# Kernel optimization log

Measured on AMD Instinct MI355X. Metric: run time of the kernel, lower is better.

Reference implementation:

```python
import jax, jax.numpy as jnp
import numpy as np

N = 100000   # nodes
E = 1600000  # edges
IN = 128     # input feature dim
C = 64       # per-layer output dim (filters)
H = 2        # attention heads
EPS = 1e-5   # batchnorm eps


def setup_inputs() -> dict:
    key = jax.random.key(0)
    ks = jax.random.split(key, 32)
    rn = lambda k, s, sc=0.05: jax.random.normal(k, s, jnp.float32) * sc
    inp = {
        "x": jax.random.normal(ks[0], (N, IN), jnp.float32),
        "edge_index": jax.random.randint(ks[1], (2, E), 0, N, jnp.int32),
        # GATConv layer 0 (IN -> C, H heads, concat=False)
        "W0": rn(ks[2], (IN, H * C)), "as0": rn(ks[3], (H, C)), "ad0": rn(ks[4], (H, C)), "b0": jnp.zeros((C,), jnp.float32),
        "skip0": rn(ks[5], (IN, C)),  # Linear(IN->C, bias=False); layers 1,2 skips are Identity
        "g0": jnp.ones((C,), jnp.float32), "be0": jnp.zeros((C,), jnp.float32),
        # GATConv layer 1 (C -> C)
        "W1": rn(ks[6], (C, H * C)), "as1": rn(ks[7], (H, C)), "ad1": rn(ks[8], (H, C)), "b1": jnp.zeros((C,), jnp.float32),
        "g1": jnp.ones((C,), jnp.float32), "be1": jnp.zeros((C,), jnp.float32),
        # GATConv layer 2 (C -> C)
        "W2": rn(ks[9], (C, H * C)), "as2": rn(ks[10], (H, C)), "ad2": rn(ks[11], (H, C)), "b2": jnp.zeros((C,), jnp.float32),
        "g2": jnp.ones((C,), jnp.float32), "be2": jnp.zeros((C,), jnp.float32),
        # JK projection for input (IN -> C, with bias); other projections are Identity
        "projW": rn(ks[12], (IN, C)), "projb": jnp.zeros((C,), jnp.float32),
    }
    return inp


def _gat(x, edge_index, W, a_src, a_dst, b):
    # PyG GATConv, concat=False: mean over heads, bias added after mean.
    h = (x @ W).reshape(-1, H, C)                 # [N, H, C]
    src, dst = edge_index[0], edge_index[1]
    e_src = jnp.sum(h * a_src, axis=-1)           # [N, H]
    e_dst = jnp.sum(h * a_dst, axis=-1)           # [N, H]
    e = jax.nn.leaky_relu(e_src[src] + e_dst[dst], 0.2)  # [E, H]
    m = jax.ops.segment_max(e, dst, num_segments=N)      # neighbor softmax (stable)
    w = jnp.exp(e - m[dst])
    denom = jax.ops.segment_sum(w, dst, num_segments=N)
    alpha = w / (denom[dst] + 1e-16)              # [E, H]
    out = jax.ops.segment_sum(alpha[:, :, None] * h[src], dst, num_segments=N)  # [N, H, C]
    return out.mean(axis=1) + b


def _bn(x, g, b):
    # BatchNorm1d, training-mode batch statistics (deterministic reference)
    mu = x.mean(axis=0)
    var = x.var(axis=0)
    return (x - mu) * jax.lax.rsqrt(var + EPS) * g + b


def reference(x, edge_index, W0, as0, ad0, b0, skip0, g0, be0,
              W1, as1, ad1, b1, g1, be1,
              W2, as2, ad2, b2, g2, be2,
              projW, projb):
    lrelu = lambda v: jax.nn.leaky_relu(v, 0.01)  # nn.LeakyReLU default
    jk0 = x @ projW + projb                       # proj_lyrs[0]
    # layer 0: GAT + projected skip, BN, (dropout=identity in eval), LeakyReLU
    h1 = _gat(x, edge_index, W0, as0, ad0, b0) + x @ skip0
    h1 = lrelu(_bn(h1, g0, be0))
    # layer 1: identity skip
    h2 = _gat(h1, edge_index, W1, as1, ad1, b1) + h1
    h2 = lrelu(_bn(h2, g1, be1))
    # layer 2: identity skip
    h3 = _gat(h2, edge_index, W2, as2, ad2, b2) + h2
    h3 = lrelu(_bn(h3, g2, be2))
    # jumping knowledge, mode='max': elementwise max over [input_proj, h1, h2, h3]
    return jnp.max(jnp.stack([jk0, h1, h2, h3], axis=0), axis=0)
```

## Files before the change

### kernel.cpp

```cpp
#include <hip/hip_runtime.h>

#define NN 100000
#define NE 1600000

constexpr int NBUC = 196;
constexpr int BIN_CHUNK = 4096;
constexpr int NB_BIN = (NE + BIN_CHUNK - 1) / BIN_CHUNK;

typedef __attribute__((ext_vector_type(8))) short s16x8;
typedef __attribute__((ext_vector_type(4))) float f32x4;
typedef __attribute__((ext_vector_type(2))) float f32x2;

__device__ inline unsigned short f2bf(float f) {
    unsigned int u = __float_as_uint(f);
    return (unsigned short)((u + 0x7fffu + ((u >> 16) & 1u)) >> 16);
}
__device__ inline float bf_lo(unsigned int pk) { return __uint_as_float(pk << 16); }
__device__ inline float bf_hi(unsigned int pk) { return __uint_as_float(pk & 0xffff0000u); }

__global__ void zero_u32(unsigned int* p, int n) {
    int i = blockIdx.x * blockDim.x + threadIdx.x;
    if (i < n) p[i] = 0u;
}

__global__ __launch_bounds__(256) void bucket_count(const int* __restrict__ dst,
                                                    int* __restrict__ bcount) {
    __shared__ int hist[NBUC];
    int t = threadIdx.x;
    for (int b = t; b < NBUC; b += 256) hist[b] = 0;
    __syncthreads();
    int beg = blockIdx.x * BIN_CHUNK;
    int end = min(beg + BIN_CHUNK, NE);
    for (int i = beg + t; i < end; i += 256) atomicAdd(&hist[dst[i] >> 9], 1);
    __syncthreads();
    for (int b = t; b < NBUC; b += 256)
        if (hist[b]) atomicAdd(&bcount[b], hist[b]);
}

__global__ void bucket_scan(const int* __restrict__ bcount, int* __restrict__ bbase,
                            int* __restrict__ bucket_cursor, int* __restrict__ offsets) {
    if (threadIdx.x == 0) {
        int run = 0;
        for (int b = 0; b < NBUC; ++b) {
            bbase[b] = run;
            bucket_cursor[b] = run;
            run += bcount[b];
        }
        bbase[NBUC] = NE;
        offsets[NN] = NE;
    }
}

__global__ __launch_bounds__(256) void bin_edges(const int* __restrict__ src,
                                                 const int* __restrict__ dst,
                                                 int* __restrict__ bucket_cursor,
                                                 unsigned int* __restrict__ binned) {
    __shared__ int hist[NBUC];
    __shared__ int base[NBUC];
    int t = threadIdx.x;
    for (int b = t; b < NBUC; b += 256) hist[b] = 0;
    __syncthreads();
    int beg = blockIdx.x * BIN_CHUNK;
    int end = min(beg + BIN_CHUNK, NE);
    for (int i = beg + t; i < end; i += 256) atomicAdd(&hist[dst[i] >> 9], 1);
    __syncthreads();
    for (int b = t; b < NBUC; b += 256) {
        base[b] = hist[b] ? atomicAdd(&bucket_cursor[b], hist[b]) : 0;
        hist[b] = 0;
    }
    __syncthreads();
    for (int i = beg + t; i < end; i += 256) {
        int d = dst[i];
        int bk = d >> 9;
        int loc = atomicAdd(&hist[bk], 1);
        binned[base[bk] + loc] = ((unsigned)(d & 511) << 17) | (unsigned)src[i];
    }
}

__global__ __launch_bounds__(256) void bucket_sort(const unsigned int* __restrict__ binned,
                                                   const int* __restrict__ bbase,
                                                   int* __restrict__ offsets,
                                                   int* __restrict__ csr_src,
                                                   int* __restrict__ csr_dst) {
    __shared__ int deg[512];
    __shared__ int loc[512];
    __shared__ int s2[256];
    int t = threadIdx.x;
    int b = blockIdx.x;
    int beg = bbase[b], end = bbase[b + 1];
    int nbase = b << 9;
    deg[t] = 0;
    deg[t + 256] = 0;
    __syncthreads();
    for (int i = beg + t; i < end; i += 256) atomicAdd(&deg[binned[i] >> 17], 1);
    __syncthreads();
    int pairsum = deg[2 * t] + deg[2 * t + 1];
    s2[t] = pairsum;
    __syncthreads();
    for (int off = 1; off < 256; off <<= 1) {
        int v = (t >= off) ? s2[t - off] : 0;
        __syncthreads();
        s2[t] += v;
        __syncthreads();
    }
    int ex = s2[t] - pairsum;
    loc[2 * t] = ex;
    loc[2 * t + 1] = ex + deg[2 * t];
    __syncthreads();
    for (int i = t; i < 512; i += 256) {
        int node = nbase + i;
        if (node < NN) offsets[node] = beg + loc[i];
    }
    __syncthreads();
    for (int i = beg + t; i < end; i += 256) {
        unsigned int v = binned[i];
        int dl = v >> 17;
        int pos = atomicAdd(&loc[dl], 1);
        csr_src[beg + pos] = (int)(v & 0x1FFFFu);
        csr_dst[beg + pos] = nbase + dl;
    }
}

__global__ void prep_weights(const float* __restrict__ W0, const float* __restrict__ skip0,
                             const float* __restrict__ projW, const float* __restrict__ W1,
                             const float* __restrict__ W2, unsigned short* __restrict__ Wtcat,
                             unsigned short* __restrict__ Wt1, unsigned short* __restrict__ Wt2) {
    int i = blockIdx.x * 256 + threadIdx.x;
    if (i < 32768) {
        int oc = i >> 7, k = i & 127;
        float v;
        if (oc < 128) v = W0[k * 128 + oc];
        else if (oc < 192) v = skip0[k * 64 + (oc - 128)];
        else v = projW[k * 64 + (oc - 192)];
        Wtcat[oc * 128 + k] = f2bf(v);
    } else if (i < 40960) {
        int j = i - 32768, oc = j >> 6, k = j & 63;
        Wt1[oc * 64 + k] = f2bf(W1[k * 128 + oc]);
    } else if (i < 49152) {
        int j = i - 40960, oc = j >> 6, k = j & 63;
        Wt2[oc * 64 + k] = f2bf(W2[k * 128 + oc]);
    }
}

template <int K, bool L0, bool XFORM>
__global__ __launch_bounds__(256) void gemm_mfma(
    const float* __restrict__ X, const unsigned short* __restrict__ Wt,
    unsigned int* __restrict__ Hq32, float* __restrict__ skipx, float* __restrict__ jkproj,
    const float* __restrict__ projb, const float* __restrict__ bnsc,
    const float* __restrict__ as_v, const float* __restrict__ ad_v,
    unsigned int* __restrict__ e_srcpk, unsigned int* __restrict__ e_dstpk) {
    constexpr int KP = K + 8;
    __shared__ unsigned short As[64 * KP];
    __shared__ unsigned short Bs[128 * KP];
    int t = threadIdx.x;
    int rbase = blockIdx.x * 64;
    const unsigned short* Wtg = Wt + (size_t)blockIdx.y * 128 * K;

    for (int i = t; i < 64 * (K / 4); i += 256) {
        int r = i / (K / 4);
        int kq = (i % (K / 4)) * 4;
        int gr = rbase + r;
        float4 v = make_float4(0.f, 0.f, 0.f, 0.f);
        if (gr < NN) {
            v = *(const float4*)&X[(size_t)gr * K + kq];
            if (XFORM) {
                float* vc = (float*)&v;
#pragma unroll
                for (int c = 0; c < 4; ++c) {
                    float val = vc[c] * bnsc[kq + c] + bnsc[64 + kq + c];
                    vc[c] = val >= 0.f ? val : 0.01f * val;
                }
            }
        }
        uint2 u;
        u.x = (unsigned int)f2bf(v.x) | ((unsigned int)f2bf(v.y) << 16);
        u.y = (unsigned int)f2bf(v.z) | ((unsigned int)f2bf(v.w) << 16);
        *(uint2*)&As[r * KP + kq] = u;
    }
    for (int i = t; i < 128 * (K / 8); i += 256) {
        int oc = i / (K / 8);
        int k8 = (i % (K / 8)) * 8;
        uint4 v = *(const uint4*)&Wtg[(size_t)oc * K + k8];
        *(uint4*)&Bs[oc * KP + k8] = v;
    }
    __syncthreads();

    int lane = t & 63, wv = t >> 6;
    int lr = lane & 15, quad = lane >> 4;
    int arow = wv * 16 + lr;
    f32x4 acc[8];
#pragma unroll
    for (int c = 0; c < 8; ++c) acc[c] = (f32x4)(0.f);
#pragma unroll
    for (int k0 = 0; k0 < K; k0 += 32) {
        s16x8 a = *(const s16x8*)&As[arow * KP + k0 + quad * 8];
#pragma unroll
        for (int ct = 0; ct < 8; ++ct) {
            s16x8 b = *(const s16x8*)&Bs[(ct * 16 + lr) * KP + k0 + quad * 8];
            acc[ct] = __builtin_amdgcn_mfma_f32_16x16x32_bf16(a, b, acc[ct], 0, 0, 0);
        }
    }

    bool hblock = (!L0) || (blockIdx.y == 0);
#pragma unroll
    for (int reg = 0; reg < 4; ++reg) {
        int row = rbase + wv * 16 + quad * 4 + reg;
        if (hblock) {
            if (row < NN) {
#pragma unroll
                for (int ct = 0; ct < 4; ++ct) {
                    int pk = __builtin_amdgcn_cvt_pk_fp8_f32(acc[ct][reg], acc[ct + 4][reg],
                                                             0, false);
                    int pn = __shfl_xor(pk, 1, 64);
                    if (!(lr & 1))
                        Hq32[(size_t)row * 32 + ct * 8 + (lr >> 1)] =
                            (unsigned int)((pk & 0xFFFF) | (pn << 16));
                }
            }
            float s0 = 0.f, s1 = 0.f, d0 = 0.f, d1 = 0.f;
#pragma unroll
            for (int ct = 0; ct < 4; ++ct) {
                int c = ct * 16 + lr;
                float hlo = acc[ct][reg], hhi = acc[ct + 4][reg];
                s0 += hlo * as_v[c];
                s1 += hhi * as_v[64 + c];
                d0 += hlo * ad_v[c];
                d1 += hhi * ad_v[64 + c];
            }
#pragma unroll
            for (int off = 1; off < 16; off <<= 1) {
                s0 += __shfl_xor(s0, off, 64);
                s1 += __shfl_xor(s1, off, 64);
                d0 += __shfl_xor(d0, off, 64);
                d1 += __shfl_xor(d1, off, 64);
            }
            if (lr == 0 && row < NN) {
                e_srcpk[row] = (unsigned int)f2bf(s0) | ((unsigned int)f2bf(s1) << 16);
                e_dstpk[row] = (unsigned int)f2bf(d0) | ((unsigned int)f2bf(d1) << 16);
            }
        } else if (row < NN) {
#pragma unroll
            for (int ct = 0; ct < 4; ++ct)
                skipx[(size_t)row * 64 + ct * 16 + lr] = acc[ct][reg];
#pragma unroll
            for (int ct = 4; ct < 8; ++ct) {
                int c = (ct - 4) * 16 + lr;
                jkproj[(size_t)row * 64 + c] = acc[ct][reg] + projb[c];
            }
        }
    }
}

__global__ void edge_w(const int* __restrict__ csr_src, const int* __restrict__ csr_dst,
                       const unsigned int* __restrict__ e_srcpk,
                       const unsigned int* __restrict__ e_dstpk,
                       uint2* __restrict__ erec) {
    int i = blockIdx.x * blockDim.x + threadIdx.x;
    if (i >= NE) return;
    int s = csr_src[i];
    unsigned int q = e_srcpk[s];
    unsigned int r = e_dstpk[csr_dst[i]];
    float a0 = bf_lo(q) + bf_lo(r);
    float a1 = bf_hi(q) + bf_hi(r);
    a0 = a0 >= 0.f ? a0 : 0.2f * a0;
    a1 = a1 >= 0.f ? a1 : 0.2f * a1;
    unsigned int w = (unsigned int)f2bf(__expf(a0)) | ((unsigned int)f2bf(__expf(a1)) << 16);
    erec[i] = make_uint2((unsigned)s, w);
}

__global__ __launch_bounds__(256) void aggregate(
    const int* __restrict__ offsets, const uint2* __restrict__ erec,
    const unsigned int* __restrict__ Hq32, const float* __restrict__ skipsrc,
    const float* __restrict__ bnsc, const float* __restrict__ bias,
    float* __restrict__ hraw) {
    int wave = threadIdx.x >> 6;
    int lane = threadIdx.x & 63;
    int n = blockIdx.x * 4 + wave;
    if (n >= NN) return;
    const unsigned char* __restrict__ Hq8 = (const unsigned char*)Hq32;
    int beg = __builtin_amdgcn_readfirstlane(offsets[n]);
    int end = __builtin_amdgcn_readfirstlane(offsets[n + 1]);
    int voff = lane * 2;

    float a0 = 0.f, a1 = 0.f, den0 = 0.f, den1 = 0.f;

    auto edge = [&](uint2 e) {
        unsigned s = (unsigned)__builtin_amdgcn_readfirstlane((int)e.x);
        unsigned w = (unsigned)__builtin_amdgcn_readfirstlane((int)e.y);
        unsigned int us = *(const unsigned short*)(Hq8 + (size_t)s * 128 + voff);
        f32x2 hv = __builtin_amdgcn_cvt_pk_f32_fp8((int)us, false);
        float w0 = bf_lo(w), w1 = bf_hi(w);
        den0 += w0;
        den1 += w1;
        a0 += w0 * hv[0];
        a1 += w1 * hv[1];
    };

    int j = beg;
    for (; j + 7 < end; j += 8) {
        uint2 e0 = erec[j + 0];
        uint2 e1 = erec[j + 1];
        uint2 e2 = erec[j + 2];
        uint2 e3 = erec[j + 3];
        uint2 e4 = erec[j + 4];
        uint2 e5 = erec[j + 5];
        uint2 e6 = erec[j + 6];
        uint2 e7 = erec[j + 7];
        edge(e0);
        edge(e1);
        edge(e2);
        edge(e3);
        edge(e4);
        edge(e5);
        edge(e6);
        edge(e7);
    }
    if (j + 3 < end) {
        uint2 e0 = erec[j + 0];
        uint2 e1 = erec[j + 1];
        uint2 e2 = erec[j + 2];
        uint2 e3 = erec[j + 3];
        edge(e0);
        edge(e1);
        edge(e2);
        edge(e3);
        j += 4;
    }
    if (j + 1 < end) {
        uint2 e0 = erec[j + 0];
        uint2 e1 = erec[j + 1];
        edge(e0);
        edge(e1);
        j += 2;
    }
    if (j < end) {
        edge(erec[j]);
    }

    float sv = skipsrc[(size_t)n * 64 + lane];
    if (bnsc) {
        sv = sv * bnsc[lane] + bnsc[64 + lane];
        sv = sv >= 0.f ? sv : 0.01f * sv;
    }
    float id0 = 1.f / (den0 + 1e-16f), id1 = 1.f / (den1 + 1e-16f);
    float o = 0.5f * (a0 * id0 + a1 * id1) + bias[lane] + sv;
    hraw[(size_t)n * 64 + lane] = o;
}

__global__ void bn_stats(const float* __restrict__ x, float* __restrict__ sums) {
    __shared__ float ls[256], ls2[256];
    int t = threadIdx.x;
    int c = t & 63, q = t >> 6;
    float s = 0.f, s2 = 0.f;
    int rbeg = blockIdx.x * 512;
    for (int r = rbeg + q; r < rbeg + 512; r += 4) {
        if (r < NN) {
            float v = x[(size_t)r * 64 + c];
            s += v;
            s2 += v * v;
        }
    }
    ls[t] = s;
    ls2[t] = s2;
    __syncthreads();
    if (t < 64) {
        s = ls[t] + ls[t + 64] + ls[t + 128] + ls[t + 192];
        s2 = ls2[t] + ls2[t + 64] + ls2[t + 128] + ls2[t + 192];
        atomicAdd(&sums[c], s);
        atomicAdd(&sums[64 + c], s2);
    }
}

__global__ void bn_final(const float* __restrict__ sums, const float* __restrict__ g,
                         const float* __restrict__ be, float* __restrict__ sc_sh) {
    int c = threadIdx.x;
    if (c < 64) {
        float mu = sums[c] / (float)NN;
        float var = sums[64 + c] / (float)NN - mu * mu;
        float sc = g[c] * rsqrtf(var + 1e-5f);
        sc_sh[c] = sc;
        sc_sh[64 + c] = be[c] - mu * sc;
    }
}

__global__ void final_out(const float* __restrict__ jkproj, const float* __restrict__ hA,
                          const float* __restrict__ hB, const float* __restrict__ hC,
                          const float* __restrict__ bnAll, float* __restrict__ out) {
    int i = blockIdx.x * blockDim.x + threadIdx.x;
    if (i < NN * 64) {
        int c = i & 63;
        float v0 = hA[i] * bnAll[c] + bnAll[64 + c];
        float v1 = hB[i] * bnAll[128 + c] + bnAll[192 + c];
        float v2 = hC[i] * bnAll[256 + c] + bnAll[320 + c];
        v0 = v0 >= 0.f ? v0 : 0.01f * v0;
        v1 = v1 >= 0.f ? v1 : 0.01f * v1;
        v2 = v2 >= 0.f ? v2 : 0.01f * v2;
        out[i] = fmaxf(fmaxf(jkproj[i], v0), fmaxf(v1, v2));
    }
}

extern "C" void kernel_launch(void* const* d_in, const int* in_sizes, int n_in,
                              void* d_out, int out_size, void* d_ws, size_t ws_size,
                              hipStream_t stream) {
    const float* x = (const float*)d_in[0];
    const int* ei = (const int*)d_in[1];
    const int* e_src_idx = ei;
    const int* e_dst_idx = ei + NE;
    const float* W0 = (const float*)d_in[2];
    const float* as0 = (const float*)d_in[3];
    const float* ad0 = (const float*)d_in[4];
    const float* b0 = (const float*)d_in[5];
    const float* skip0 = (const float*)d_in[6];
    const float* g0 = (const float*)d_in[7];
    const float* be0 = (const float*)d_in[8];
    const float* W1 = (const float*)d_in[9];
    const float* as1 = (const float*)d_in[10];
    const float* ad1 = (const float*)d_in[11];
    const float* b1 = (const float*)d_in[12];
    const float* g1 = (const float*)d_in[13];
    const float* be1 = (const float*)d_in[14];
    const float* W2 = (const float*)d_in[15];
    const float* as2 = (const float*)d_in[16];
    const float* ad2 = (const float*)d_in[17];
    const float* b2 = (const float*)d_in[18];
    const float* g2 = (const float*)d_in[19];
    const float* be2 = (const float*)d_in[20];
    const float* projW = (const float*)d_in[21];
    const float* projb = (const float*)d_in[22];
    float* out = (float*)d_out;

    char* p = (char*)d_ws;
    auto alloc = [&](size_t bytes) {
        char* r = p;
        p += (bytes + 255) & ~(size_t)255;
        return r;
    };
    int* zbuf = (int*)alloc((size_t)(196 + 384) * 4);
    int* bcount = zbuf;
    float* bnsumAll = (float*)(zbuf + 196);
    int* bbase = (int*)alloc((size_t)(NBUC + 1) * 4);
    int* bucket_cursor = (int*)alloc((size_t)NBUC * 4);
    int* offsets = (int*)alloc((size_t)(NN + 1) * 4);
    int* csr_src = (int*)alloc((size_t)NE * 4);
    int* csr_dst = (int*)alloc((size_t)NE * 4);
    uint2* erec = (uint2*)alloc((size_t)NE * 8);
    unsigned int* binned = (unsigned int*)alloc((size_t)NE * 4);
    unsigned int* h_q32 = (unsigned int*)alloc((size_t)NN * 32 * 4);
    unsigned int* e_srcpk = (unsigned int*)alloc((size_t)NN * 4);
    unsigned int* e_dstpk = (unsigned int*)alloc((size_t)NN * 4);
    float* skipx = (float*)alloc((size_t)NN * 64 * 4);
    float* jkproj = (float*)alloc((size_t)NN * 64 * 4);
    float* hrawA = (float*)alloc((size_t)NN * 64 * 4);
    float* hrawB = (float*)alloc((size_t)NN * 64 * 4);
    float* hrawC = (float*)alloc((size_t)NN * 64 * 4);
    unsigned short* Wtcat = (unsigned short*)alloc(256 * 128 * 2);
    unsigned short* Wt1 = (unsigned short*)alloc(128 * 64 * 2);
    unsigned short* Wt2 = (unsigned short*)alloc(128 * 64 * 2);
    float* bnscAll = (float*)alloc(3 * 128 * 4);
    if ((size_t)(p - (char*)d_ws) > ws_size) return;

    zero_u32<<<3, 256, 0, stream>>>((unsigned int*)zbuf, 196 + 384);
    bucket_count<<<NB_BIN, 256, 0, stream>>>(e_dst_idx, bcount);
    bucket_scan<<<1, 64, 0, stream>>>(bcount, bbase, bucket_cursor, offsets);
    bin_edges<<<NB_BIN, 256, 0, stream>>>(e_src_idx, e_dst_idx, bucket_cursor, binned);
    bucket_sort<<<NBUC, 256, 0, stream>>>(binned, bbase, offsets, csr_src, csr_dst);
    prep_weights<<<192, 256, 0, stream>>>(W0, skip0, projW, W1, W2, Wtcat, Wt1, Wt2);

    int gblocks = (NN + 63) / 64;

    gemm_mfma<128, true, false><<<dim3(gblocks, 2), 256, 0, stream>>>(
        x, Wtcat, h_q32, skipx, jkproj, projb, nullptr, as0, ad0, e_srcpk, e_dstpk);
    edge_w<<<(NE + 255) / 256, 256, 0, stream>>>(csr_src, csr_dst, e_srcpk, e_dstpk, erec);
    aggregate<<<(NN + 3) / 4, 256, 0, stream>>>(offsets, erec, h_q32, skipx, nullptr, b0,
                                                hrawA);
    bn_stats<<<(NN + 511) / 512, 256, 0, stream>>>(hrawA, bnsumAll);
    bn_final<<<1, 64, 0, stream>>>(bnsumAll, g0, be0, bnscAll);

    gemm_mfma<64, false, true><<<dim3(gblocks, 1), 256, 0, stream>>>(
        hrawA, Wt1, h_q32, nullptr, nullptr, nullptr, bnscAll, as1, ad1, e_srcpk, e_dstpk);
    edge_w<<<(NE + 255) / 256, 256, 0, stream>>>(csr_src, csr_dst, e_srcpk, e_dstpk, erec);
    aggregate<<<(NN + 3) / 4, 256, 0, stream>>>(offsets, erec, h_q32, hrawA, bnscAll, b1,
                                                hrawB);
    bn_stats<<<(NN + 511) / 512, 256, 0, stream>>>(hrawB, bnsumAll + 128);
    bn_final<<<1, 64, 0, stream>>>(bnsumAll + 128, g1, be1, bnscAll + 128);

    gemm_mfma<64, false, true><<<dim3(gblocks, 1), 256, 0, stream>>>(
        hrawB, Wt2, h_q32, nullptr, nullptr, nullptr, bnscAll + 128, as2, ad2, e_srcpk,
        e_dstpk);
    edge_w<<<(NE + 255) / 256, 256, 0, stream>>>(csr_src, csr_dst, e_srcpk, e_dstpk, erec);
    aggregate<<<(NN + 3) / 4, 256, 0, stream>>>(offsets, erec, h_q32, hrawB, bnscAll + 128,
                                                b2, hrawC);
    bn_stats<<<(NN + 511) / 512, 256, 0, stream>>>(hrawC, bnsumAll + 256);
    bn_final<<<1, 64, 0, stream>>>(bnsumAll + 256, g2, be2, bnscAll + 256);

    final_out<<<(NN * 64 + 255) / 256, 256, 0, stream>>>(jkproj, hrawA, hrawB, hrawC,
                                                         bnscAll, out);
}
```

Before: 601.1 us.

## Fuse edge attention weights into aggregation and fold attention vectors into GEMM

```diff
diff --git a/kernel.cpp b/kernel.cpp
--- a/kernel.cpp
+++ b/kernel.cpp
@@ -10,6 +10,11 @@
 typedef __attribute__((ext_vector_type(8))) short s16x8;
 typedef __attribute__((ext_vector_type(4))) float f32x4;
 typedef __attribute__((ext_vector_type(2))) float f32x2;
+
+template <int M>
+struct IC {
+    static constexpr int value = M;
+};
 
 __device__ inline unsigned short f2bf(float f) {
     unsigned int u = __float_as_uint(f);
@@ -80,8 +85,7 @@
 __global__ __launch_bounds__(256) void bucket_sort(const unsigned int* __restrict__ binned,
                                                    const int* __restrict__ bbase,
                                                    int* __restrict__ offsets,
-                                                   int* __restrict__ csr_src,
-                                                   int* __restrict__ csr_dst) {
+                                                   int* __restrict__ csr_src) {
     __shared__ int deg[512];
     __shared__ int loc[512];
     __shared__ int s2[256];
@@ -117,28 +121,60 @@
         int dl = v >> 17;
         int pos = atomicAdd(&loc[dl], 1);
         csr_src[beg + pos] = (int)(v & 0x1FFFFu);
-        csr_dst[beg + pos] = nbase + dl;
     }
 }
 
 __global__ void prep_weights(const float* __restrict__ W0, const float* __restrict__ skip0,
                              const float* __restrict__ projW, const float* __restrict__ W1,
-                             const float* __restrict__ W2, unsigned short* __restrict__ Wtcat,
-                             unsigned short* __restrict__ Wt1, unsigned short* __restrict__ Wt2) {
+                             const float* __restrict__ W2,
+                             const float* __restrict__ as0, const float* __restrict__ ad0,
+                             const float* __restrict__ as1, const float* __restrict__ ad1,
+                             const float* __restrict__ as2, const float* __restrict__ ad2,
+                             unsigned short* __restrict__ Wtcat,
+                             unsigned short* __restrict__ Wt1,
+                             unsigned short* __restrict__ Wt2) {
     int i = blockIdx.x * 256 + threadIdx.x;
-    if (i < 32768) {
+    if (i < 16384) {
         int oc = i >> 7, k = i & 127;
-        float v;
-        if (oc < 128) v = W0[k * 128 + oc];
-        else if (oc < 192) v = skip0[k * 64 + (oc - 128)];
-        else v = projW[k * 64 + (oc - 192)];
-        Wtcat[oc * 128 + k] = f2bf(v);
+        Wtcat[oc * 128 + k] = f2bf(W0[k * 128 + oc]);
+    } else if (i < 32768) {
+        int j = i - 16384;
+        int oc = j >> 7, k = j & 127;
+        float v = (oc < 64) ? skip0[k * 64 + oc] : projW[k * 64 + (oc - 64)];
+        Wtcat[132 * 128 + oc * 128 + k] = f2bf(v);
     } else if (i < 40960) {
         int j = i - 32768, oc = j >> 6, k = j & 63;
         Wt1[oc * 64 + k] = f2bf(W1[k * 128 + oc]);
     } else if (i < 49152) {
         int j = i - 40960, oc = j >> 6, k = j & 63;
         Wt2[oc * 64 + k] = f2bf(W2[k * 128 + oc]);
+    } else if (i < 50688) {
+        int e = i - 49152;
+        if (e < 512) {
+            int k = e >> 2, sc = e & 3, head = sc & 1;
+            const float* av = (sc < 2 ? as0 : ad0) + head * 64;
+            const float* wr = W0 + k * 128 + head * 64;
+            float s = 0.f;
+            for (int c = 0; c < 64; ++c) s += wr[c] * av[c];
+            Wtcat[(128 + sc) * 128 + k] = f2bf(s);
+        } else if (e < 1024) {
+            int j = e - 512, k = j >> 2, sc = j & 3;
+            Wtcat[132 * 128 + (128 + sc) * 128 + k] = 0;
+        } else if (e < 1280) {
+            int j = e - 1024, k = j >> 2, sc = j & 3, head = sc & 1;
+            const float* av = (sc < 2 ? as1 : ad1) + head * 64;
+            const float* wr = W1 + k * 128 + head * 64;
+            float s = 0.f;
+            for (int c = 0; c < 64; ++c) s += wr[c] * av[c];
+            Wt1[(128 + sc) * 64 + k] = f2bf(s);
+        } else {
+            int j = e - 1280, k = j >> 2, sc = j & 3, head = sc & 1;
+            const float* av = (sc < 2 ? as2 : ad2) + head * 64;
+            const float* wr = W2 + k * 128 + head * 64;
+            float s = 0.f;
+            for (int c = 0; c < 64; ++c) s += wr[c] * av[c];
+            Wt2[(128 + sc) * 64 + k] = f2bf(s);
+        }
     }
 }
 
@@ -147,14 +183,14 @@
     const float* __restrict__ X, const unsigned short* __restrict__ Wt,
     unsigned int* __restrict__ Hq32, float* __restrict__ skipx, float* __restrict__ jkproj,
     const float* __restrict__ projb, const float* __restrict__ bnsc,
-    const float* __restrict__ as_v, const float* __restrict__ ad_v,
     unsigned int* __restrict__ e_srcpk, unsigned int* __restrict__ e_dstpk) {
     constexpr int KP = K + 8;
+    constexpr int NC = 132;
     __shared__ unsigned short As[64 * KP];
-    __shared__ unsigned short Bs[128 * KP];
+    __shared__ unsigned short Bs[NC * KP];
     int t = threadIdx.x;
     int rbase = blockIdx.x * 64;
-    const unsigned short* Wtg = Wt + (size_t)blockIdx.y * 128 * K;
+    const unsigned short* Wtg = Wt + (size_t)blockIdx.y * NC * K;
 
     for (int i = t; i < 64 * (K / 4); i += 256) {
         int r = i / (K / 4);
@@ -177,7 +213,7 @@
         u.y = (unsigned int)f2bf(v.z) | ((unsigned int)f2bf(v.w) << 16);
         *(uint2*)&As[r * KP + kq] = u;
     }
-    for (int i = t; i < 128 * (K / 8); i += 256) {
+    for (int i = t; i < NC * (K / 8); i += 256) {
         int oc = i / (K / 8);
         int k8 = (i % (K / 8)) * 8;
         uint4 v = *(const uint4*)&Wtg[(size_t)oc * K + k8];
@@ -189,6 +225,7 @@
     int lr = lane & 15, quad = lane >> 4;
     int arow = wv * 16 + lr;
     f32x4 acc[8];
+    f32x4 acc8 = (f32x4)(0.f);
 #pragma unroll
     for (int c = 0; c < 8; ++c) acc[c] = (f32x4)(0.f);
 #pragma unroll
@@ -199,6 +236,8 @@
             s16x8 b = *(const s16x8*)&Bs[(ct * 16 + lr) * KP + k0 + quad * 8];
             acc[ct] = __builtin_amdgcn_mfma_f32_16x16x32_bf16(a, b, acc[ct], 0, 0, 0);
         }
+        s16x8 b9 = *(const s16x8*)&Bs[(128 + (lr & 3)) * KP + k0 + quad * 8];
+        acc8 = __builtin_amdgcn_mfma_f32_16x16x32_bf16(a, b9, acc8, 0, 0, 0);
     }
 
     bool hblock = (!L0) || (blockIdx.y == 0);
@@ -217,26 +256,12 @@
                             (unsigned int)((pk & 0xFFFF) | (pn << 16));
                 }
             }
-            float s0 = 0.f, s1 = 0.f, d0 = 0.f, d1 = 0.f;
-#pragma unroll
-            for (int ct = 0; ct < 4; ++ct) {
-                int c = ct * 16 + lr;
-                float hlo = acc[ct][reg], hhi = acc[ct + 4][reg];
-                s0 += hlo * as_v[c];
-                s1 += hhi * as_v[64 + c];
-                d0 += hlo * ad_v[c];
-                d1 += hhi * ad_v[64 + c];
-            }
-#pragma unroll
-            for (int off = 1; off < 16; off <<= 1) {
-                s0 += __shfl_xor(s0, off, 64);
-                s1 += __shfl_xor(s1, off, 64);
-                d0 += __shfl_xor(d0, off, 64);
-                d1 += __shfl_xor(d1, off, 64);
-            }
-            if (lr == 0 && row < NN) {
-                e_srcpk[row] = (unsigned int)f2bf(s0) | ((unsigned int)f2bf(s1) << 16);
-                e_dstpk[row] = (unsigned int)f2bf(d0) | ((unsigned int)f2bf(d1) << 16);
+            float own = acc8[reg];
+            float par = __shfl_xor(own, 1, 64);
+            if (row < NN) {
+                unsigned int pkv = (unsigned)f2bf(own) | ((unsigned)f2bf(par) << 16);
+                if (lr == 0) e_srcpk[row] = pkv;
+                else if (lr == 2) e_dstpk[row] = pkv;
             }
         } else if (row < NN) {
 #pragma unroll
@@ -251,25 +276,9 @@
     }
 }
 
-__global__ void edge_w(const int* __restrict__ csr_src, const int* __restrict__ csr_dst,
-                       const unsigned int* __restrict__ e_srcpk,
-                       const unsigned int* __restrict__ e_dstpk,
-                       uint2* __restrict__ erec) {
-    int i = blockIdx.x * blockDim.x + threadIdx.x;
-    if (i >= NE) return;
-    int s = csr_src[i];
-    unsigned int q = e_srcpk[s];
-    unsigned int r = e_dstpk[csr_dst[i]];
-    float a0 = bf_lo(q) + bf_lo(r);
-    float a1 = bf_hi(q) + bf_hi(r);
-    a0 = a0 >= 0.f ? a0 : 0.2f * a0;
-    a1 = a1 >= 0.f ? a1 : 0.2f * a1;
-    unsigned int w = (unsigned int)f2bf(__expf(a0)) | ((unsigned int)f2bf(__expf(a1)) << 16);
-    erec[i] = make_uint2((unsigned)s, w);
-}
-
 __global__ __launch_bounds__(256) void aggregate(
-    const int* __restrict__ offsets, const uint2* __restrict__ erec,
+    const int* __restrict__ offsets, const int* __restrict__ csr_src,
+    const unsigned int* __restrict__ e_srcpk, const unsigned int* __restrict__ e_dstpk,
     const unsigned int* __restrict__ Hq32, const float* __restrict__ skipsrc,
     const float* __restrict__ bnsc, const float* __restrict__ bias,
     float* __restrict__ hraw) {
@@ -280,62 +289,46 @@
     const unsigned char* __restrict__ Hq8 = (const unsigned char*)Hq32;
     int beg = __builtin_amdgcn_readfirstlane(offsets[n]);
     int end = __builtin_amdgcn_readfirstlane(offsets[n + 1]);
+    unsigned qd = (unsigned)__builtin_amdgcn_readfirstlane((int)e_dstpk[n]);
+    float dd0 = bf_lo(qd), dd1 = bf_hi(qd);
     int voff = lane * 2;
 
     float a0 = 0.f, a1 = 0.f, den0 = 0.f, den1 = 0.f;
-
-    auto edge = [&](uint2 e) {
-        unsigned s = (unsigned)__builtin_amdgcn_readfirstlane((int)e.x);
-        unsigned w = (unsigned)__builtin_amdgcn_readfirstlane((int)e.y);
-        unsigned int us = *(const unsigned short*)(Hq8 + (size_t)s * 128 + voff);
-        f32x2 hv = __builtin_amdgcn_cvt_pk_f32_fp8((int)us, false);
-        float w0 = bf_lo(w), w1 = bf_hi(w);
-        den0 += w0;
-        den1 += w1;
-        a0 += w0 * hv[0];
-        a1 += w1 * hv[1];
+    int j = beg;
+
+    auto batch = [&](auto Mc) {
+        constexpr int M = decltype(Mc)::value;
+        int ss[M];
+        unsigned qq[M];
+        unsigned short uu[M];
+#pragma unroll
+        for (int u = 0; u < M; ++u)
+            ss[u] = __builtin_amdgcn_readfirstlane(csr_src[j + u]);
+#pragma unroll
+        for (int u = 0; u < M; ++u)
+            qq[u] = (unsigned)__builtin_amdgcn_readfirstlane((int)e_srcpk[ss[u]]);
+#pragma unroll
+        for (int u = 0; u < M; ++u)
+            uu[u] = *(const unsigned short*)(Hq8 + (size_t)ss[u] * 128 + voff);
+#pragma unroll
+        for (int u = 0; u < M; ++u) {
+            float e0 = bf_lo(qq[u]) + dd0, e1 = bf_hi(qq[u]) + dd1;
+            e0 = e0 >= 0.f ? e0 : 0.2f * e0;
+            e1 = e1 >= 0.f ? e1 : 0.2f * e1;
+            float w0 = __expf(e0), w1 = __expf(e1);
+            f32x2 hv = __builtin_amdgcn_cvt_pk_f32_fp8((int)uu[u], false);
+            den0 += w0;
+            den1 += w1;
+            a0 += w0 * hv[0];
+            a1 += w1 * hv[1];
+        }
+        j += M;
     };
 
-    int j = beg;
-    for (; j + 7 < end; j += 8) {
-        uint2 e0 = erec[j + 0];
-        uint2 e1 = erec[j + 1];
-        uint2 e2 = erec[j + 2];
-        uint2 e3 = erec[j + 3];
-        uint2 e4 = erec[j + 4];
-        uint2 e5 = erec[j + 5];
-        uint2 e6 = erec[j + 6];
-        uint2 e7 = erec[j + 7];
-        edge(e0);
-        edge(e1);
-        edge(e2);
-        edge(e3);
-        edge(e4);
-        edge(e5);
-        edge(e6);
-        edge(e7);
-    }
-    if (j + 3 < end) {
-        uint2 e0 = erec[j + 0];
-        uint2 e1 = erec[j + 1];
-        uint2 e2 = erec[j + 2];
-        uint2 e3 = erec[j + 3];
-        edge(e0);
-        edge(e1);
-        edge(e2);
-        edge(e3);
-        j += 4;
-    }
-    if (j + 1 < end) {
-        uint2 e0 = erec[j + 0];
-        uint2 e1 = erec[j + 1];
-        edge(e0);
-        edge(e1);
-        j += 2;
-    }
-    if (j < end) {
-        edge(erec[j]);
-    }
+    while (j + 8 <= end) batch(IC<8>{});
+    if (j + 4 <= end) batch(IC<4>{});
+    if (j + 2 <= end) batch(IC<2>{});
+    if (j < end) batch(IC<1>{});
 
     float sv = skipsrc[(size_t)n * 64 + lane];
     if (bnsc) {
@@ -442,8 +435,6 @@
     int* bucket_cursor = (int*)alloc((size_t)NBUC * 4);
     int* offsets = (int*)alloc((size_t)(NN + 1) * 4);
     int* csr_src = (int*)alloc((size_t)NE * 4);
-    int* csr_dst = (int*)alloc((size_t)NE * 4);
-    uint2* erec = (uint2*)alloc((size_t)NE * 8);
     unsigned int* binned = (unsigned int*)alloc((size_t)NE * 4);
     unsigned int* h_q32 = (unsigned int*)alloc((size_t)NN * 32 * 4);
     unsigned int* e_srcpk = (unsigned int*)alloc((size_t)NN * 4);
@@ -453,9 +444,9 @@
     float* hrawA = (float*)alloc((size_t)NN * 64 * 4);
     float* hrawB = (float*)alloc((size_t)NN * 64 * 4);
     float* hrawC = (float*)alloc((size_t)NN * 64 * 4);
-    unsigned short* Wtcat = (unsigned short*)alloc(256 * 128 * 2);
-    unsigned short* Wt1 = (unsigned short*)alloc(128 * 64 * 2);
-    unsigned short* Wt2 = (unsigned short*)alloc(128 * 64 * 2);
+    unsigned short* Wtcat = (unsigned short*)alloc((size_t)2 * 132 * 128 * 2);
+    unsigned short* Wt1 = (unsigned short*)alloc((size_t)132 * 64 * 2);
+    unsigned short* Wt2 = (unsigned short*)alloc((size_t)132 * 64 * 2);
     float* bnscAll = (float*)alloc(3 * 128 * 4);
     if ((size_t)(p - (char*)d_ws) > ws_size) return;
 
@@ -463,33 +454,30 @@
     bucket_count<<<NB_BIN, 256, 0, stream>>>(e_dst_idx, bcount);
     bucket_scan<<<1, 64, 0, stream>>>(bcount, bbase, bucket_cursor, offsets);
     bin_edges<<<NB_BIN, 256, 0, stream>>>(e_src_idx, e_dst_idx, bucket_cursor, binned);
-    bucket_sort<<<NBUC, 256, 0, stream>>>(binned, bbase, offsets, csr_src, csr_dst);
-    prep_weights<<<192, 256, 0, stream>>>(W0, skip0, projW, W1, W2, Wtcat, Wt1, Wt2);
+    bucket_sort<<<NBUC, 256, 0, stream>>>(binned, bbase, offsets, csr_src);
+    prep_weights<<<198, 256, 0, stream>>>(W0, skip0, projW, W1, W2, as0, ad0, as1, ad1,
+                                          as2, ad2, Wtcat, Wt1, Wt2);
 
     int gblocks = (NN + 63) / 64;
 
     gemm_mfma<128, true, false><<<dim3(gblocks, 2), 256, 0, stream>>>(
-        x, Wtcat, h_q32, skipx, jkproj, projb, nullptr, as0, ad0, e_srcpk, e_dstpk);
-    edge_w<<<(NE + 255) / 256, 256, 0, stream>>>(csr_src, csr_dst, e_srcpk, e_dstpk, erec);
-    aggregate<<<(NN + 3) / 4, 256, 0, stream>>>(offsets, erec, h_q32, skipx, nullptr, b0,
-                                                hrawA);
+        x, Wtcat, h_q32, skipx, jkproj, projb, nullptr, e_srcpk, e_dstpk);
+    aggregate<<<(NN + 3) / 4, 256, 0, stream>>>(offsets, csr_src, e_srcpk, e_dstpk, h_q32,
+                                                skipx, nullptr, b0, hrawA);
     bn_stats<<<(NN + 511) / 512, 256, 0, stream>>>(hrawA, bnsumAll);
     bn_final<<<1, 64, 0, stream>>>(bnsumAll, g0, be0, bnscAll);
 
     gemm_mfma<64, false, true><<<dim3(gblocks, 1), 256, 0, stream>>>(
-        hrawA, Wt1, h_q32, nullptr, nullptr, nullptr, bnscAll, as1, ad1, e_srcpk, e_dstpk);
-    edge_w<<<(NE + 255) / 256, 256, 0, stream>>>(csr_src, csr_dst, e_srcpk, e_dstpk, erec);
-    aggregate<<<(NN + 3) / 4, 256, 0, stream>>>(offsets, erec, h_q32, hrawA, bnscAll, b1,
-                                                hrawB);
+        hrawA, Wt1, h_q32, nullptr, nullptr, nullptr, bnscAll, e_srcpk, e_dstpk);
+    aggregate<<<(NN + 3) / 4, 256, 0, stream>>>(offsets, csr_src, e_srcpk, e_dstpk, h_q32,
+                                                hrawA, bnscAll, b1, hrawB);
     bn_stats<<<(NN + 511) / 512, 256, 0, stream>>>(hrawB, bnsumAll + 128);
     bn_final<<<1, 64, 0, stream>>>(bnsumAll + 128, g1, be1, bnscAll + 128);
 
     gemm_mfma<64, false, true><<<dim3(gblocks, 1), 256, 0, stream>>>(
-        hrawB, Wt2, h_q32, nullptr, nullptr, nullptr, bnscAll + 128, as2, ad2, e_srcpk,
-        e_dstpk);
-    edge_w<<<(NE + 255) / 256, 256, 0, stream>>>(csr_src, csr_dst, e_srcpk, e_dstpk, erec);
-    aggregate<<<(NN + 3) / 4, 256, 0, stream>>>(offsets, erec, h_q32, hrawB, bnscAll + 128,
-                                                b2, hrawC);
+        hrawB, Wt2, h_q32, nullptr, nullptr, nullptr, bnscAll + 128, e_srcpk, e_dstpk);
+    aggregate<<<(NN + 3) / 4, 256, 0, stream>>>(offsets, csr_src, e_srcpk, e_dstpk, h_q32,
+                                                hrawB, bnscAll + 128, b2, hrawC);
     bn_stats<<<(NN + 511) / 512, 256, 0, stream>>>(hrawC, bnsumAll + 256);
     bn_final<<<1, 64, 0, stream>>>(bnsumAll + 256, g2, be2, bnscAll + 256);
 
```

Measured after the change: 635.3 us. 5.7% more time.
